# Kernel optimization log

Measured on AMD Instinct MI355X. Metric: run time of the kernel, lower is better.

## Reference

```python
import jax, jax.numpy as jnp
import numpy as np

N, NFEAT, NHID = 10000, 128, 64


def _gc(x, adj, W, b):
    # GraphConvolution: adj @ (x @ W) + b
    return adj @ (x @ W) + b


def _fwd(x, adj, Wg0, bg0, Wg1, bg1, Wt0, bt0, Wt1, bt1,
         W000, b000, W001, b001, W100, b100, W101, b101,
         Wo0, bo0, Wo1, bo1, Wpp, bpp, Wpp2, bpp2, a, t):
    H = Wg0.shape[1]
    # outcome GCN stack (n_in=2), dropout is eval no-op
    rep_o = jax.nn.relu(_gc(x, adj, Wg0, bg0))
    rep_o = jax.nn.relu(_gc(rep_o, adj, Wg1, bg1))
    # treatment GCN stack
    rep_t = jax.nn.relu(_gc(x, adj, Wt0, bt0))
    rep_t = jax.nn.relu(_gc(rep_t, adj, Wt1, bt1))

    rep_cat = jnp.concatenate([rep_o, rep_t], axis=1)  # [N, 2H]
    # edge score(i,j) = [rep_cat_i ; rep_cat_j] @ a  =  s_src_i + s_dst_j
    s_src = rep_cat @ a[:2 * H, 0]   # [N]
    s_dst = rep_cat @ a[2 * H:, 0]   # [N]
    scores = s_src[:, None] + s_dst[None, :]          # [N, N]
    # only nonzero adj entries get a score; rest remain 0 (index_put into zeros)
    att = jnp.where(adj != 0, scores, jnp.zeros((), scores.dtype))
    att = jax.nn.softmax(att, axis=1)                 # full dense row softmax

    rep_out = att @ rep_t + rep_o                     # [N, H]

    treatment = jax.nn.sigmoid((rep_t @ Wpp + bpp) @ Wpp2 + bpp2)  # [N, 2]

    rep0 = rep_out
    rep1 = rep_out
    y00 = jax.nn.relu(rep0 @ W000 + b000)
    y10 = jax.nn.relu(rep1 @ W100 + b100)
    y00 = jax.nn.relu(y00 @ W001 + b001)
    y10 = jax.nn.relu(y10 @ W101 + b101)
    y0 = (y00 @ Wo0 + bo0).reshape(-1)
    y1 = (y10 @ Wo1 + bo1).reshape(-1)
    y = jnp.where(t > 0, y1, y0)
    return (y, rep_out, treatment)


def setup_inputs() -> dict:
    key = jax.random.key(0)
    ks = jax.random.split(key, 32)
    H = NHID
    x = jax.random.normal(ks[0], (N, NFEAT), dtype=jnp.float32)
    u = jax.random.uniform(ks[1], (N, N), dtype=jnp.float32)
    adj = jnp.where(u < 0.002, u, jnp.zeros((), jnp.float32))
    t = jax.random.randint(ks[2], (N,), 0, 2, dtype=jnp.int32)

    def lin(k, fi, fo):
        s = 1.0 / np.sqrt(fi)
        kw, kb = jax.random.split(k)
        return (jax.random.uniform(kw, (fi, fo), jnp.float32, -s, s),
                jax.random.uniform(kb, (fo,), jnp.float32, -s, s))

    Wg0, bg0 = lin(ks[3], NFEAT, H)
    Wg1, bg1 = lin(ks[4], H, H)
    Wt0, bt0 = lin(ks[5], NFEAT, H)
    Wt1, bt1 = lin(ks[6], H, H)
    W000, b000 = lin(ks[7], H, H)
    W001, b001 = lin(ks[8], H, H)
    W100, b100 = lin(ks[9], H, H)
    W101, b101 = lin(ks[10], H, H)
    Wo0, bo0 = lin(ks[11], H, 1)
    Wo1, bo1 = lin(ks[12], H, 1)
    Wpp, bpp = lin(ks[13], H, H)
    Wpp2, bpp2 = lin(ks[14], H, 2)
    # torch init is xavier with gain=0 (all zeros); use small random for a
    # meaningful correctness baseline
    a = jax.random.normal(ks[15], (4 * H, 1), dtype=jnp.float32) * 0.1
    return dict(x=x, adj=adj, t=t,
                Wg0=Wg0, bg0=bg0, Wg1=Wg1, bg1=bg1,
                Wt0=Wt0, bt0=bt0, Wt1=Wt1, bt1=bt1,
                W000=W000, b000=b000, W001=W001, b001=b001,
                W100=W100, b100=b100, W101=W101, b101=b101,
                Wo0=Wo0, bo0=bo0, Wo1=Wo1, bo1=bo1,
                Wpp=Wpp, bpp=bpp, Wpp2=Wpp2, bpp2=bpp2, a=a)


def reference(x, adj, t, Wg0, bg0, Wg1, bg1, Wt0, bt0, Wt1, bt1,
              W000, b000, W001, b001, W100, b100, W101, b101,
              Wo0, bo0, Wo1, bo1, Wpp, bpp, Wpp2, bpp2, a):
    return _fwd(x, adj, Wg0, bg0, Wg1, bg1, Wt0, bt0, Wt1, bt1,
                W000, b000, W001, b001, W100, b100, W101, b101,
                Wo0, bo0, Wo1, bo1, Wpp, bpp, Wpp2, bpp2, a, t)
```

## Files before the change

### kernel.cpp

```cpp
#include <hip/hip_runtime.h>
#include <hip/hip_bf16.h>

#define N_NODES 10000
#define ROW4    2500
#define CAP     64
#define SPAR_BLOCKS 2500
#define TOTAL_K1    3750

typedef float fx4 __attribute__((ext_vector_type(4)));

#define OFF_CNT     0
#define OFF_COLSUM  10000
#define OFF_SSRC    10064
#define OFF_SDST    20064
#define OFF_PAIRS   30064
#define OFF_PQ      1310064
#define OFF_REPO    1310064
#define OFF_REPT    1950064
#define OFF_PQ2     2590064

__device__ __forceinline__ float wave_sum(float v) {
    #pragma unroll
    for (int off = 32; off >= 1; off >>= 1) v += __shfl_xor(v, off, 64);
    return v;
}
__device__ __forceinline__ float wave_max(float v) {
    #pragma unroll
    for (int off = 32; off >= 1; off >>= 1) v = fmaxf(v, __shfl_xor(v, off, 64));
    return v;
}

__global__ void k1_fused(const fx4* __restrict__ adj4, const float* __restrict__ x,
                         const float* __restrict__ Wg0, const float* __restrict__ Wt0,
                         int* __restrict__ cnt, float2* __restrict__ pairs,
                         float* __restrict__ colsum,
                         float* __restrict__ PQ) {
    __shared__ float xs[8 * 128];
    int tid = threadIdx.x;
    if (blockIdx.x < SPAR_BLOCKS) {
        int lane = tid & 63, w = tid >> 6;
        int row = (SPAR_BLOCKS - 1 - (int)blockIdx.x) * 4 + w;
        if (blockIdx.x == 0 && tid < 64) colsum[tid] = 0.0f;
        const fx4* rp = adj4 + (size_t)row * ROW4;
        size_t base = (size_t)row * CAP;
        int count = 0;
        for (int it = 0; it < 40; it += 8) {
            fx4 v[8];
            #pragma unroll
            for (int j = 0; j < 8; ++j) {
                int idx = (it + j) * 64 + lane;
                v[j] = (fx4){0.f, 0.f, 0.f, 0.f};
                if (idx < ROW4) v[j] = __builtin_nontemporal_load(rp + idx);
            }
            #pragma unroll
            for (int j = 0; j < 8; ++j) {
                int idx = (it + j) * 64 + lane;
                float vv[4] = {v[j].x, v[j].y, v[j].z, v[j].w};
                bool any = (vv[0] != 0.f) | (vv[1] != 0.f) | (vv[2] != 0.f) | (vv[3] != 0.f);
                if (__ballot(any)) {
                    #pragma unroll
                    for (int l = 0; l < 4; ++l) {
                        unsigned long long b = __ballot(vv[l] != 0.f);
                        if (b) {
                            int pre = __popcll(b & ((1ull << lane) - 1ull));
                            if (vv[l] != 0.f) {
                                int pos = count + pre;
                                if (pos < CAP)
                                    pairs[base + pos] =
                                        make_float2(__int_as_float(idx * 4 + l), vv[l]);
                            }
                            count += (int)__popcll(b);
                        }
                    }
                }
            }
        }
        if (lane == 0) cnt[row] = min(count, CAP);
    } else {
        int row0 = (blockIdx.x - SPAR_BLOCKS) * 8;
        ((float4*)xs)[tid] = ((const float4*)(x + (size_t)row0 * 128))[tid];
        __syncthreads();
        int sub = tid >> 6, f = tid & 63;
        #pragma unroll
        for (int g = 0; g < 2; ++g) {
            const float* xr = xs + (g * 4 + sub) * 128;
            float aP = 0.0f, aQ = 0.0f;
            #pragma unroll 8
            for (int k = 0; k < 128; k += 4) {
                float4 xv = *(const float4*)(xr + k);
                aP += xv.x * Wg0[(k + 0) * 64 + f] + xv.y * Wg0[(k + 1) * 64 + f]
                    + xv.z * Wg0[(k + 2) * 64 + f] + xv.w * Wg0[(k + 3) * 64 + f];
                aQ += xv.x * Wt0[(k + 0) * 64 + f] + xv.y * Wt0[(k + 1) * 64 + f]
                    + xv.z * Wt0[(k + 2) * 64 + f] + xv.w * Wt0[(k + 3) * 64 + f];
            }
            *(float2*)(PQ + (size_t)(row0 + g * 4 + sub) * 128 + 2 * f) =
                make_float2(aP, aQ);
        }
    }
}

__device__ __forceinline__ void gather16_f2(const float* __restrict__ SRC,
                                            int c, float v_l, int c_l, int f,
                                            float& accA, float& accB) {
    float a0 = 0.f, a1 = 0.f, b0 = 0.f, b1 = 0.f;
    for (int p = 0; p < c; p += 16) {
        float vv[16]; int cc[16];
        #pragma unroll
        for (int j = 0; j < 16; ++j) {
            vv[j] = __shfl(v_l, p + j, 64);
            cc[j] = __shfl(c_l, p + j, 64);
        }
        float2 pq[16];
        #pragma unroll
        for (int j = 0; j < 16; ++j)
            pq[j] = *(const float2*)(SRC + (size_t)cc[j] * 128 + 2 * f);
        #pragma unroll
        for (int j = 0; j < 16; j += 2) {
            a0 += vv[j] * pq[j].x;     b0 += vv[j] * pq[j].y;
            a1 += vv[j + 1] * pq[j + 1].x; b1 += vv[j + 1] * pq[j + 1].y;
        }
    }
    accA = a0 + a1;
    accB = b0 + b1;
}

__global__ void k2_agg_gemm(const int* __restrict__ cnt, const float2* __restrict__ pairs,
                            const float* __restrict__ PQ,
                            const float* __restrict__ bg0, const float* __restrict__ bt0,
                            const float* __restrict__ Wg1, const float* __restrict__ Wt1,
                            float* __restrict__ PQ2) {
    __shared__ float ra[8 * 64], rb[8 * 64];
    int tid = threadIdx.x, row0 = blockIdx.x * 8, sub = tid >> 6, f = tid & 63;
    float bo = bg0[f], bt = bt0[f];
    #pragma unroll
    for (int g = 0; g < 2; ++g) {
        int lr = g * 4 + sub, row = row0 + lr;
        int c = min(cnt[row], CAP);
        float2 pr = make_float2(0.f, 0.f);
        if (f < c) pr = pairs[(size_t)row * CAP + f];
        int c_l = __float_as_int(pr.x); float v_l = pr.y;
        float aA, aB;
        gather16_f2(PQ, c, v_l, c_l, f, aA, aB);
        ra[lr * 64 + f] = fmaxf(aA + bo, 0.0f);
        rb[lr * 64 + f] = fmaxf(aB + bt, 0.0f);
    }
    __syncthreads();
    #pragma unroll
    for (int g = 0; g < 2; ++g) {
        int lr = g * 4 + sub, row = row0 + lr;
        const float* rra = ra + lr * 64;
        const float* rrb = rb + lr * 64;
        float aA = 0.f, aB = 0.f;
        #pragma unroll 8
        for (int k = 0; k < 64; k += 4) {
            float4 va = *(const float4*)(rra + k);
            float4 vb = *(const float4*)(rrb + k);
            aA += va.x * Wg1[(k + 0) * 64 + f] + va.y * Wg1[(k + 1) * 64 + f]
                + va.z * Wg1[(k + 2) * 64 + f] + va.w * Wg1[(k + 3) * 64 + f];
            aB += vb.x * Wt1[(k + 0) * 64 + f] + vb.y * Wt1[(k + 1) * 64 + f]
                + vb.z * Wt1[(k + 2) * 64 + f] + vb.w * Wt1[(k + 3) * 64 + f];
        }
        *(float2*)(PQ2 + (size_t)row * 128 + 2 * f) = make_float2(aA, aB);
    }
}

__global__ void k3_agg_score(const int* __restrict__ cnt, const float2* __restrict__ pairs,
                             const float* __restrict__ PQ2,
                             const float* __restrict__ bg1, const float* __restrict__ bt1,
                             const float* __restrict__ a,
                             const float* __restrict__ Wpp, const float* __restrict__ bpp,
                             const float* __restrict__ Wpp2, const float* __restrict__ bpp2,
                             float* __restrict__ rep_o, float* __restrict__ rep_t,
                             float* __restrict__ s_src, float* __restrict__ s_dst,
                             float* __restrict__ colsum, float* __restrict__ out_trt) {
    __shared__ float rts[8 * 64];
    int tid = threadIdx.x, row0 = blockIdx.x * 8, sub = tid >> 6, f = tid & 63;
    float bo = bg1[f], bt = bt1[f];
    float a0c = a[f], a1c = a[64 + f], a2c = a[128 + f], a3c = a[192 + f];
    #pragma unroll
    for (int g = 0; g < 2; ++g) {
        int lr = g * 4 + sub, row = row0 + lr;
        int c = min(cnt[row], CAP);
        float2 pr = make_float2(0.f, 0.f);
        if (f < c) pr = pairs[(size_t)row * CAP + f];
        int c_l = __float_as_int(pr.x); float v_l = pr.y;
        float aA, aB;
        gather16_f2(PQ2, c, v_l, c_l, f, aA, aB);
        float vo = fmaxf(aA + bo, 0.0f);
        float vt = fmaxf(aB + bt, 0.0f);
        rep_o[(size_t)row * 64 + f] = vo;
        rep_t[(size_t)row * 64 + f] = vt;
        rts[lr * 64 + f] = vt;
        float ps = wave_sum(vo * a0c + vt * a1c);
        float pd = wave_sum(vo * a2c + vt * a3c);
        if (f == 0) { s_src[row] = ps; s_dst[row] = pd; }
    }
    __syncthreads();
    if (sub == 0) {
        float cs = 0.0f;
        #pragma unroll
        for (int lr = 0; lr < 8; ++lr) cs += rts[lr * 64 + f];
        atomicAdd(&colsum[f], cs);
    }
    float bp = bpp[f], w20 = Wpp2[f * 2 + 0], w21 = Wpp2[f * 2 + 1];
    #pragma unroll
    for (int g = 0; g < 2; ++g) {
        int lr = g * 4 + sub, row = row0 + lr;
        const float* rr = rts + lr * 64;
        float u = bp;
        #pragma unroll 8
        for (int k = 0; k < 64; k += 4) {
            float4 rv = *(const float4*)(rr + k);
            u += rv.x * Wpp[(k + 0) * 64 + f] + rv.y * Wpp[(k + 1) * 64 + f]
               + rv.z * Wpp[(k + 2) * 64 + f] + rv.w * Wpp[(k + 3) * 64 + f];
        }
        float p0 = wave_sum(u * w20);
        float p1 = wave_sum(u * w21);
        if (f == 0) {
            out_trt[(size_t)row * 2 + 0] = 1.0f / (1.0f + expf(-(p0 + bpp2[0])));
            out_trt[(size_t)row * 2 + 1] = 1.0f / (1.0f + expf(-(p1 + bpp2[1])));
        }
    }
}

__global__ void k4_attn_heads(const int* __restrict__ cnt, const float2* __restrict__ pairs,
                              const float* __restrict__ s_src, const float* __restrict__ s_dst,
                              const float* __restrict__ colsum,
                              const float* __restrict__ rep_o, const float* __restrict__ rep_t,
                              const float* __restrict__ W000, const float* __restrict__ b000,
                              const float* __restrict__ W001, const float* __restrict__ b001,
                              const float* __restrict__ W100, const float* __restrict__ b100,
                              const float* __restrict__ W101, const float* __restrict__ b101,
                              const float* __restrict__ Wo0, const float* __restrict__ bo0,
                              const float* __restrict__ Wo1, const float* __restrict__ bo1,
                              const int* __restrict__ t,
                              float* __restrict__ out_y, float* __restrict__ out_rep) {
    __shared__ float reps[8 * 64], u0s[8 * 64], u1s[8 * 64];
    int tid = threadIdx.x, row0 = blockIdx.x * 8, sub = tid >> 6, f = tid & 63;
    float csf = colsum[f];
    #pragma unroll
    for (int g = 0; g < 2; ++g) {
        int lr = g * 4 + sub, row = row0 + lr;
        int c = min(cnt[row], CAP);
        float ssrc = s_src[row];
        int   col_l = (f < c) ? __float_as_int(pairs[(size_t)row * CAP + f].x) : 0;
        float s_l   = (f < c) ? ssrc + s_dst[col_l] : -1e30f;
        float m = fmaxf(wave_max(s_l), 0.0f);
        float e_l = (f < c) ? expf(s_l - m) : 0.0f;
        float em = expf(-m);
        float Z = wave_sum(e_l) + (float)(N_NODES - c) * em;
        float g_l = (f < c) ? (e_l - em) : 0.0f;
        float acc0 = 0.f, acc1 = 0.f;
        for (int p = 0; p < c; p += 16) {
            float gg[16]; int cc[16];
            #pragma unroll
            for (int j = 0; j < 16; ++j) {
                gg[j] = __shfl(g_l, p + j, 64);
                cc[j] = __shfl(col_l, p + j, 64);
            }
            float rt[16];
            #pragma unroll
            for (int j = 0; j < 16; ++j)
                rt[j] = rep_t[(size_t)cc[j] * 64 + f];
            #pragma unroll
            for (int j = 0; j < 16; j += 2) {
                acc0 += gg[j] * rt[j];
                acc1 += gg[j + 1] * rt[j + 1];
            }
        }
        float outv = ((acc0 + acc1) + em * csf) / Z + rep_o[(size_t)row * 64 + f];
        out_rep[(size_t)row * 64 + f] = outv;
        reps[lr * 64 + f] = outv;
    }
    __syncthreads();
    float bA = b000[f], bB = b100[f];
    #pragma unroll
    for (int g = 0; g < 2; ++g) {
        int lr = g * 4 + sub;
        const float* rr = reps + lr * 64;
        float u0 = bA, u1 = bB;
        #pragma unroll 8
        for (int k = 0; k < 64; k += 4) {
            float4 rv = *(const float4*)(rr + k);
            u0 += rv.x * W000[(k + 0) * 64 + f] + rv.y * W000[(k + 1) * 64 + f]
                + rv.z * W000[(k + 2) * 64 + f] + rv.w * W000[(k + 3) * 64 + f];
            u1 += rv.x * W100[(k + 0) * 64 + f] + rv.y * W100[(k + 1) * 64 + f]
                + rv.z * W100[(k + 2) * 64 + f] + rv.w * W100[(k + 3) * 64 + f];
        }
        u0s[lr * 64 + f] = fmaxf(u0, 0.0f);
        u1s[lr * 64 + f] = fmaxf(u1, 0.0f);
    }
    __syncthreads();
    float bC = b001[f], bD = b101[f], wo0 = Wo0[f], wo1 = Wo1[f];
    #pragma unroll
    for (int g = 0; g < 2; ++g) {
        int lr = g * 4 + sub, row = row0 + lr;
        const float* r0 = u0s + lr * 64;
        const float* r1 = u1s + lr * 64;
        float v0 = bC, v1 = bD;
        #pragma unroll 8
        for (int k = 0; k < 64; k += 4) {
            float4 q0 = *(const float4*)(r0 + k);
            float4 q1 = *(const float4*)(r1 + k);
            v0 += q0.x * W001[(k + 0) * 64 + f] + q0.y * W001[(k + 1) * 64 + f]
                + q0.z * W001[(k + 2) * 64 + f] + q0.w * W001[(k + 3) * 64 + f];
            v1 += q1.x * W101[(k + 0) * 64 + f] + q1.y * W101[(k + 1) * 64 + f]
                + q1.z * W101[(k + 2) * 64 + f] + q1.w * W101[(k + 3) * 64 + f];
        }
        float y0 = wave_sum(fmaxf(v0, 0.0f) * wo0);
        float y1 = wave_sum(fmaxf(v1, 0.0f) * wo1);
        if (f == 0)
            out_y[row] = (t[row] > 0) ? (y1 + bo1[0]) : (y0 + bo0[0]);
    }
}


extern "C" void kernel_launch(void* const* d_in, const int* in_sizes, int n_in,
                              void* d_out, int out_size, void* d_ws, size_t ws_size,
                              hipStream_t stream) {
    const float* x    = (const float*)d_in[0];
    const float* adj  = (const float*)d_in[1];
    const int*   t    = (const int*)d_in[2];
    const float* Wg0  = (const float*)d_in[3];
    const float* bg0  = (const float*)d_in[4];
    const float* Wg1  = (const float*)d_in[5];
    const float* bg1  = (const float*)d_in[6];
    const float* Wt0  = (const float*)d_in[7];
    const float* bt0  = (const float*)d_in[8];
    const float* Wt1  = (const float*)d_in[9];
    const float* bt1  = (const float*)d_in[10];
    const float* W000 = (const float*)d_in[11];
    const float* b000 = (const float*)d_in[12];
    const float* W001 = (const float*)d_in[13];
    const float* b001 = (const float*)d_in[14];
    const float* W100 = (const float*)d_in[15];
    const float* b100 = (const float*)d_in[16];
    const float* W101 = (const float*)d_in[17];
    const float* b101 = (const float*)d_in[18];
    const float* Wo0  = (const float*)d_in[19];
    const float* bo0  = (const float*)d_in[20];
    const float* Wo1  = (const float*)d_in[21];
    const float* bo1  = (const float*)d_in[22];
    const float* Wpp  = (const float*)d_in[23];
    const float* bpp  = (const float*)d_in[24];
    const float* Wpp2 = (const float*)d_in[25];
    const float* bpp2 = (const float*)d_in[26];
    const float* a    = (const float*)d_in[27];

    float* ws = (float*)d_ws;
    int*    cnt    = (int*)(ws + OFF_CNT);
    float*  colsum = ws + OFF_COLSUM;
    float*  s_src  = ws + OFF_SSRC;
    float*  s_dst  = ws + OFF_SDST;
    float2* pairs  = (float2*)(ws + OFF_PAIRS);
    float*  PQ     = ws + OFF_PQ;
    float*  PQ2    = ws + OFF_PQ2;
    float*  rep_o  = ws + OFF_REPO;
    float*  rep_t  = ws + OFF_REPT;

    float* out_y   = (float*)d_out;
    float* out_rep = (float*)d_out + N_NODES;
    float* out_trt = (float*)d_out + N_NODES + N_NODES * 64;

    k1_fused<<<TOTAL_K1, 256, 0, stream>>>((const fx4*)adj, x, Wg0, Wt0,
                                           cnt, pairs, colsum, PQ);
    k2_agg_gemm<<<1250, 256, 0, stream>>>(cnt, pairs, PQ, bg0, bt0, Wg1, Wt1, PQ2);
    k3_agg_score<<<1250, 256, 0, stream>>>(cnt, pairs, PQ2, bg1, bt1, a,
                                           Wpp, bpp, Wpp2, bpp2,
                                           rep_o, rep_t, s_src, s_dst, colsum, out_trt);
    k4_attn_heads<<<1250, 256, 0, stream>>>(cnt, pairs, s_src, s_dst, colsum, rep_o, rep_t,
                                            W000, b000, W001, b001,
                                            W100, b100, W101, b101,
                                            Wo0, bo0, Wo1, bo1, t, out_y, out_rep);
}
```

Measured before the change: 656.5 us.

## Fuse adjacency scan with first aggregation and second-layer GEMM

The x@W GEMM is split out into its own small first kernel. The dense adjacency scan is fused with the first sparse aggregation and the layer-1 GEMM: each wave compacts its row's nonzeros into shared memory, writes them out, then immediately gathers PQ rows and applies Wg1/Wt1. This removes the separate k2 launch and the global round trip of reading pairs back. The cost is that the GEMM no longer overlaps with the bandwidth-bound scan, and blocks now hold only 4 rows with an 8-wide gather.

```diff
diff --git a/kernel.cpp b/kernel.cpp
--- a/kernel.cpp
+++ b/kernel.cpp
@@ -4,8 +4,7 @@
 #define N_NODES 10000
 #define ROW4    2500
 #define CAP     64
-#define SPAR_BLOCKS 2500
-#define TOTAL_K1    3750
+#define KB_BLOCKS 2500
 
 typedef float fx4 __attribute__((ext_vector_type(4)));
 
@@ -30,73 +29,29 @@
     return v;
 }
 
-__global__ void k1_fused(const fx4* __restrict__ adj4, const float* __restrict__ x,
-                         const float* __restrict__ Wg0, const float* __restrict__ Wt0,
-                         int* __restrict__ cnt, float2* __restrict__ pairs,
-                         float* __restrict__ colsum,
-                         float* __restrict__ PQ) {
-    __shared__ float xs[8 * 128];
-    int tid = threadIdx.x;
-    if (blockIdx.x < SPAR_BLOCKS) {
-        int lane = tid & 63, w = tid >> 6;
-        int row = (SPAR_BLOCKS - 1 - (int)blockIdx.x) * 4 + w;
-        if (blockIdx.x == 0 && tid < 64) colsum[tid] = 0.0f;
-        const fx4* rp = adj4 + (size_t)row * ROW4;
-        size_t base = (size_t)row * CAP;
-        int count = 0;
-        for (int it = 0; it < 40; it += 8) {
-            fx4 v[8];
-            #pragma unroll
-            for (int j = 0; j < 8; ++j) {
-                int idx = (it + j) * 64 + lane;
-                v[j] = (fx4){0.f, 0.f, 0.f, 0.f};
-                if (idx < ROW4) v[j] = __builtin_nontemporal_load(rp + idx);
-            }
-            #pragma unroll
-            for (int j = 0; j < 8; ++j) {
-                int idx = (it + j) * 64 + lane;
-                float vv[4] = {v[j].x, v[j].y, v[j].z, v[j].w};
-                bool any = (vv[0] != 0.f) | (vv[1] != 0.f) | (vv[2] != 0.f) | (vv[3] != 0.f);
-                if (__ballot(any)) {
-                    #pragma unroll
-                    for (int l = 0; l < 4; ++l) {
-                        unsigned long long b = __ballot(vv[l] != 0.f);
-                        if (b) {
-                            int pre = __popcll(b & ((1ull << lane) - 1ull));
-                            if (vv[l] != 0.f) {
-                                int pos = count + pre;
-                                if (pos < CAP)
-                                    pairs[base + pos] =
-                                        make_float2(__int_as_float(idx * 4 + l), vv[l]);
-                            }
-                            count += (int)__popcll(b);
-                        }
-                    }
-                }
-            }
-        }
-        if (lane == 0) cnt[row] = min(count, CAP);
-    } else {
-        int row0 = (blockIdx.x - SPAR_BLOCKS) * 8;
-        ((float4*)xs)[tid] = ((const float4*)(x + (size_t)row0 * 128))[tid];
-        __syncthreads();
-        int sub = tid >> 6, f = tid & 63;
-        #pragma unroll
-        for (int g = 0; g < 2; ++g) {
-            const float* xr = xs + (g * 4 + sub) * 128;
-            float aP = 0.0f, aQ = 0.0f;
-            #pragma unroll 8
-            for (int k = 0; k < 128; k += 4) {
-                float4 xv = *(const float4*)(xr + k);
-                aP += xv.x * Wg0[(k + 0) * 64 + f] + xv.y * Wg0[(k + 1) * 64 + f]
-                    + xv.z * Wg0[(k + 2) * 64 + f] + xv.w * Wg0[(k + 3) * 64 + f];
-                aQ += xv.x * Wt0[(k + 0) * 64 + f] + xv.y * Wt0[(k + 1) * 64 + f]
-                    + xv.z * Wt0[(k + 2) * 64 + f] + xv.w * Wt0[(k + 3) * 64 + f];
-            }
-            *(float2*)(PQ + (size_t)(row0 + g * 4 + sub) * 128 + 2 * f) =
-                make_float2(aP, aQ);
-        }
-    }
+__device__ __forceinline__ void gather8_f2(const float* __restrict__ SRC,
+                                           int c, float v_l, int c_l, int f,
+                                           float& accA, float& accB) {
+    float a0 = 0.f, a1 = 0.f, b0 = 0.f, b1 = 0.f;
+    for (int p = 0; p < c; p += 8) {
+        float vv[8]; int cc[8];
+        #pragma unroll
+        for (int j = 0; j < 8; ++j) {
+            vv[j] = __shfl(v_l, p + j, 64);
+            cc[j] = __shfl(c_l, p + j, 64);
+        }
+        float2 pq[8];
+        #pragma unroll
+        for (int j = 0; j < 8; ++j)
+            pq[j] = *(const float2*)(SRC + (size_t)cc[j] * 128 + 2 * f);
+        #pragma unroll
+        for (int j = 0; j < 8; j += 2) {
+            a0 += vv[j] * pq[j].x;         b0 += vv[j] * pq[j].y;
+            a1 += vv[j + 1] * pq[j + 1].x; b1 += vv[j + 1] * pq[j + 1].y;
+        }
+    }
+    accA = a0 + a1;
+    accB = b0 + b1;
 }
 
 __device__ __forceinline__ void gather16_f2(const float* __restrict__ SRC,
@@ -116,7 +71,7 @@
             pq[j] = *(const float2*)(SRC + (size_t)cc[j] * 128 + 2 * f);
         #pragma unroll
         for (int j = 0; j < 16; j += 2) {
-            a0 += vv[j] * pq[j].x;     b0 += vv[j] * pq[j].y;
+            a0 += vv[j] * pq[j].x;         b0 += vv[j] * pq[j].y;
             a1 += vv[j + 1] * pq[j + 1].x; b1 += vv[j + 1] * pq[j + 1].y;
         }
     }
@@ -124,47 +79,105 @@
     accB = b0 + b1;
 }
 
-__global__ void k2_agg_gemm(const int* __restrict__ cnt, const float2* __restrict__ pairs,
+__global__ void kA_gemm(const float* __restrict__ x,
+                        const float* __restrict__ Wg0, const float* __restrict__ Wt0,
+                        float* __restrict__ PQ, float* __restrict__ colsum) {
+    __shared__ float xs[8 * 128];
+    int tid = threadIdx.x;
+    if (blockIdx.x == 0 && tid < 64) colsum[tid] = 0.0f;
+    int row0 = blockIdx.x * 8;
+    ((float4*)xs)[tid] = ((const float4*)(x + (size_t)row0 * 128))[tid];
+    __syncthreads();
+    int sub = tid >> 6, f = tid & 63;
+    #pragma unroll
+    for (int g = 0; g < 2; ++g) {
+        const float* xr = xs + (g * 4 + sub) * 128;
+        float aP = 0.0f, aQ = 0.0f;
+        #pragma unroll 8
+        for (int k = 0; k < 128; k += 4) {
+            float4 xv = *(const float4*)(xr + k);
+            aP += xv.x * Wg0[(k + 0) * 64 + f] + xv.y * Wg0[(k + 1) * 64 + f]
+                + xv.z * Wg0[(k + 2) * 64 + f] + xv.w * Wg0[(k + 3) * 64 + f];
+            aQ += xv.x * Wt0[(k + 0) * 64 + f] + xv.y * Wt0[(k + 1) * 64 + f]
+                + xv.z * Wt0[(k + 2) * 64 + f] + xv.w * Wt0[(k + 3) * 64 + f];
+        }
+        *(float2*)(PQ + (size_t)(row0 + g * 4 + sub) * 128 + 2 * f) =
+            make_float2(aP, aQ);
+    }
+}
+
+__global__ void kB_scan_agg(const fx4* __restrict__ adj4,
                             const float* __restrict__ PQ,
                             const float* __restrict__ bg0, const float* __restrict__ bt0,
                             const float* __restrict__ Wg1, const float* __restrict__ Wt1,
+                            int* __restrict__ cnt, float2* __restrict__ pairs,
                             float* __restrict__ PQ2) {
-    __shared__ float ra[8 * 64], rb[8 * 64];
-    int tid = threadIdx.x, row0 = blockIdx.x * 8, sub = tid >> 6, f = tid & 63;
-    float bo = bg0[f], bt = bt0[f];
-    #pragma unroll
-    for (int g = 0; g < 2; ++g) {
-        int lr = g * 4 + sub, row = row0 + lr;
-        int c = min(cnt[row], CAP);
-        float2 pr = make_float2(0.f, 0.f);
-        if (f < c) pr = pairs[(size_t)row * CAP + f];
-        int c_l = __float_as_int(pr.x); float v_l = pr.y;
-        float aA, aB;
-        gather16_f2(PQ, c, v_l, c_l, f, aA, aB);
-        ra[lr * 64 + f] = fmaxf(aA + bo, 0.0f);
-        rb[lr * 64 + f] = fmaxf(aB + bt, 0.0f);
-    }
-    __syncthreads();
-    #pragma unroll
-    for (int g = 0; g < 2; ++g) {
-        int lr = g * 4 + sub, row = row0 + lr;
-        const float* rra = ra + lr * 64;
-        const float* rrb = rb + lr * 64;
-        float aA = 0.f, aB = 0.f;
-        #pragma unroll 8
-        for (int k = 0; k < 64; k += 4) {
-            float4 va = *(const float4*)(rra + k);
-            float4 vb = *(const float4*)(rrb + k);
-            aA += va.x * Wg1[(k + 0) * 64 + f] + va.y * Wg1[(k + 1) * 64 + f]
-                + va.z * Wg1[(k + 2) * 64 + f] + va.w * Wg1[(k + 3) * 64 + f];
-            aB += vb.x * Wt1[(k + 0) * 64 + f] + vb.y * Wt1[(k + 1) * 64 + f]
-                + vb.z * Wt1[(k + 2) * 64 + f] + vb.w * Wt1[(k + 3) * 64 + f];
-        }
-        *(float2*)(PQ2 + (size_t)row * 128 + 2 * f) = make_float2(aA, aB);
-    }
-}
-
-__global__ void k3_agg_score(const int* __restrict__ cnt, const float2* __restrict__ pairs,
+    __shared__ float2 lp[4][64];
+    __shared__ float ra[4 * 64], rb[4 * 64];
+    int tid = threadIdx.x, lane = tid & 63, w = tid >> 6;
+    int row = (KB_BLOCKS - 1 - (int)blockIdx.x) * 4 + w;
+    const fx4* rp = adj4 + (size_t)row * ROW4;
+    size_t base = (size_t)row * CAP;
+    int count = 0;
+    for (int it = 0; it < 40; it += 8) {
+        fx4 v[8];
+        #pragma unroll
+        for (int j = 0; j < 8; ++j) {
+            int idx = (it + j) * 64 + lane;
+            v[j] = (fx4){0.f, 0.f, 0.f, 0.f};
+            if (idx < ROW4) v[j] = __builtin_nontemporal_load(rp + idx);
+        }
+        #pragma unroll
+        for (int j = 0; j < 8; ++j) {
+            int idx = (it + j) * 64 + lane;
+            float vv[4] = {v[j].x, v[j].y, v[j].z, v[j].w};
+            bool any = (vv[0] != 0.f) | (vv[1] != 0.f) | (vv[2] != 0.f) | (vv[3] != 0.f);
+            if (__ballot(any)) {
+                #pragma unroll
+                for (int l = 0; l < 4; ++l) {
+                    unsigned long long b = __ballot(vv[l] != 0.f);
+                    if (b) {
+                        int pre = __popcll(b & ((1ull << lane) - 1ull));
+                        if (vv[l] != 0.f) {
+                            int pos = count + pre;
+                            if (pos < CAP)
+                                lp[w][pos] = make_float2(__int_as_float(idx * 4 + l), vv[l]);
+                        }
+                        count += (int)__popcll(b);
+                    }
+                }
+            }
+        }
+    }
+    int c = min(count, CAP);
+    __syncthreads();
+    int f = lane;
+    float2 pr = make_float2(0.f, 0.f);
+    if (f < c) pr = lp[w][f];
+    if (f < c) pairs[base + f] = pr;
+    if (f == 0) cnt[row] = c;
+    int c_l = __float_as_int(pr.x); float v_l = pr.y;
+    float aA, aB;
+    gather8_f2(PQ, c, v_l, c_l, f, aA, aB);
+    ra[w * 64 + f] = fmaxf(aA + bg0[f], 0.0f);
+    rb[w * 64 + f] = fmaxf(aB + bt0[f], 0.0f);
+    __syncthreads();
+    const float* rra = ra + w * 64;
+    const float* rrb = rb + w * 64;
+    float xA = 0.f, xB = 0.f;
+    #pragma unroll 8
+    for (int k = 0; k < 64; k += 4) {
+        float4 va = *(const float4*)(rra + k);
+        float4 vb = *(const float4*)(rrb + k);
+        xA += va.x * Wg1[(k + 0) * 64 + f] + va.y * Wg1[(k + 1) * 64 + f]
+            + va.z * Wg1[(k + 2) * 64 + f] + va.w * Wg1[(k + 3) * 64 + f];
+        xB += vb.x * Wt1[(k + 0) * 64 + f] + vb.y * Wt1[(k + 1) * 64 + f]
+            + vb.z * Wt1[(k + 2) * 64 + f] + vb.w * Wt1[(k + 3) * 64 + f];
+    }
+    *(float2*)(PQ2 + (size_t)row * 128 + 2 * f) = make_float2(xA, xB);
+}
+
+__global__ void kC_agg_score(const int* __restrict__ cnt, const float2* __restrict__ pairs,
                              const float* __restrict__ PQ2,
                              const float* __restrict__ bg1, const float* __restrict__ bt1,
                              const float* __restrict__ a,
@@ -223,7 +236,7 @@
     }
 }
 
-__global__ void k4_attn_heads(const int* __restrict__ cnt, const float2* __restrict__ pairs,
+__global__ void kD_attn_heads(const int* __restrict__ cnt, const float2* __restrict__ pairs,
                               const float* __restrict__ s_src, const float* __restrict__ s_dst,
                               const float* __restrict__ colsum,
                               const float* __restrict__ rep_o, const float* __restrict__ rep_t,
@@ -362,13 +375,13 @@
     float* out_rep = (float*)d_out + N_NODES;
     float* out_trt = (float*)d_out + N_NODES + N_NODES * 64;
 
-    k1_fused<<<TOTAL_K1, 256, 0, stream>>>((const fx4*)adj, x, Wg0, Wt0,
-                                           cnt, pairs, colsum, PQ);
-    k2_agg_gemm<<<1250, 256, 0, stream>>>(cnt, pairs, PQ, bg0, bt0, Wg1, Wt1, PQ2);
-    k3_agg_score<<<1250, 256, 0, stream>>>(cnt, pairs, PQ2, bg1, bt1, a,
+    kA_gemm<<<1250, 256, 0, stream>>>(x, Wg0, Wt0, PQ, colsum);
+    kB_scan_agg<<<KB_BLOCKS, 256, 0, stream>>>((const fx4*)adj, PQ, bg0, bt0,
+                                               Wg1, Wt1, cnt, pairs, PQ2);
+    kC_agg_score<<<1250, 256, 0, stream>>>(cnt, pairs, PQ2, bg1, bt1, a,
                                            Wpp, bpp, Wpp2, bpp2,
                                            rep_o, rep_t, s_src, s_dst, colsum, out_trt);
-    k4_attn_heads<<<1250, 256, 0, stream>>>(cnt, pairs, s_src, s_dst, colsum, rep_o, rep_t,
+    kD_attn_heads<<<1250, 256, 0, stream>>>(cnt, pairs, s_src, s_dst, colsum, rep_o, rep_t,
                                             W000, b000, W001, b001,
                                             W100, b100, W101, b101,
                                             Wo0, bo0, Wo1, bo1, t, out_y, out_rep);
```

Result: no change. 656.0 us (-0.1%).
